# Optimization experiments

Measured on AMD Instinct MI355X. Metric: run time of the kernel, lower is better.

Reference implementation:

```python
import jax, jax.numpy as jnp
import numpy as np

N = 50000
E = 800000
F_IN = 128
HID = 60
CAT = 3 * HID
NUM_CLASSES = 7
EPS = 1e-5


def _gcn_norm(edge_index, n):
    # add self loops, symmetric normalization (PyG gcn_norm default)
    loops = jnp.arange(n, dtype=edge_index.dtype)
    src = jnp.concatenate([edge_index[0], loops])
    dst = jnp.concatenate([edge_index[1], loops])
    deg = jax.ops.segment_sum(jnp.ones_like(src, dtype=jnp.float32), dst, num_segments=n)
    dinv = jnp.where(deg > 0, jax.lax.rsqrt(jnp.maximum(deg, 1.0)), 0.0)
    norm = dinv[src] * dinv[dst]  # [E+N]
    return src, dst, norm


def _prop(x, src, dst, norm, n):
    # sum_{j in N(i)} norm_ij * x_j
    return jax.ops.segment_sum(x[src] * norm[:, None], dst, num_segments=n)


def _mixhop(x, src, dst, norm, n, ws, bs):
    outs = [x @ ws[0] + bs[0]]  # power 0
    h = x
    for w, b in zip(ws[1:], bs[1:]):  # powers 1, 2
        h = _prop(h, src, dst, norm, n)
        outs.append(h @ w + b)
    return jnp.concatenate(outs, axis=-1)


def _batchnorm(x, g, b):
    # training-mode batch stats over node dim (biased variance, eps=1e-5)
    mu = x.mean(axis=0)
    var = x.var(axis=0)
    return (x - mu) * jax.lax.rsqrt(var + EPS) * g + b


def setup_inputs() -> dict:
    key = jax.random.key(0)
    ks = jax.random.split(key, 16)
    x = jax.random.normal(ks[0], (N, F_IN), dtype=jnp.float32)
    edge_index = jax.random.randint(ks[1], (2, E), 0, N, dtype=jnp.int64)
    def lin(k, fi, fo):
        s = 1.0 / np.sqrt(fi)
        return jax.random.uniform(k, (fi, fo), jnp.float32, -s, s)
    inp = {"x": x, "edge_index": edge_index}
    for i, p in enumerate(range(3)):
        inp[f"c1_w{p}"] = lin(ks[2 + p], F_IN, HID)
        inp[f"c1_b{p}"] = jnp.zeros((HID,), jnp.float32)
        inp[f"c2_w{p}"] = lin(ks[5 + p], CAT, HID)
        inp[f"c2_b{p}"] = jnp.zeros((HID,), jnp.float32)
        inp[f"c3_w{p}"] = lin(ks[8 + p], CAT, HID)
        inp[f"c3_b{p}"] = jnp.zeros((HID,), jnp.float32)
    for i in (1, 2, 3):
        inp[f"bn{i}_g"] = jnp.ones((CAT,), jnp.float32)
        inp[f"bn{i}_b"] = jnp.zeros((CAT,), jnp.float32)
    inp["lin_w"] = lin(ks[11], CAT, NUM_CLASSES)
    inp["lin_b"] = jnp.zeros((NUM_CLASSES,), jnp.float32)
    return inp


def reference(x, edge_index,
              c1_w0, c1_b0, c1_w1, c1_b1, c1_w2, c1_b2,
              c2_w0, c2_b0, c2_w1, c2_b1, c2_w2, c2_b2,
              c3_w0, c3_b0, c3_w1, c3_b1, c3_w2, c3_b2,
              bn1_g, bn1_b, bn2_g, bn2_b, bn3_g, bn3_b,
              lin_w, lin_b):
    n = x.shape[0]
    src, dst, norm = _gcn_norm(edge_index, n)
    # dropout layers are identity in eval mode
    h = _mixhop(x, src, dst, norm, n, (c1_w0, c1_w1, c1_w2), (c1_b0, c1_b1, c1_b2))
    h = _batchnorm(h, bn1_g, bn1_b)
    h = _mixhop(h, src, dst, norm, n, (c2_w0, c2_w1, c2_w2), (c2_b0, c2_b1, c2_b2))
    h = _batchnorm(h, bn2_g, bn2_b)
    h = _mixhop(h, src, dst, norm, n, (c3_w0, c3_w1, c3_w2), (c3_b0, c3_b1, c3_b2))
    h = _batchnorm(h, bn3_g, bn3_b)
    return h @ lin_w + lin_b
```

## Files before the change

kernel.cpp:

```cpp
#include <hip/hip_runtime.h>
#include <hip/hip_bf16.h>

#define NN 50000
#define NE 800000
#define FIN0 128
#define HID 60
#define CAT 180
#define NCLS 7
#define BN_EPS 1e-5f
#define NBUCK 196
#define BCAP 5120
#define STG 96

typedef unsigned int uint;
typedef unsigned short ushort;
typedef __attribute__((ext_vector_type(8))) short short8;
typedef __attribute__((ext_vector_type(4))) float f32x4;

__device__ __forceinline__ ushort f2bf(float f) {
    uint u = __float_as_uint(f);
    u += 0x7FFFu + ((u >> 16) & 1u);
    return (ushort)(u >> 16);
}
__device__ __forceinline__ float bf_lo(uint v) { return __uint_as_float(v << 16); }
__device__ __forceinline__ float bf_hi(uint v) { return __uint_as_float(v & 0xFFFF0000u); }
__device__ __forceinline__ float bf2f(ushort u) { return __uint_as_float(((uint)u) << 16); }


__global__ void k_initcur(int* __restrict__ gcur) {
    int t = threadIdx.x;
    if (t < NBUCK) gcur[t] = t * BCAP;
}

__global__ __launch_bounds__(256) void k_bin(const int* __restrict__ src,
                                             const int* __restrict__ dst,
                                             int* __restrict__ gcur,
                                             uint* __restrict__ ebuf, int e) {
    __shared__ int cnt[NBUCK];
    __shared__ int base[NBUCK];
    int t = threadIdx.x;
    for (int c0 = blockIdx.x * 2048; c0 < e; c0 += gridDim.x * 2048) {
        if (t < NBUCK) cnt[t] = 0;
        __syncthreads();
        uint pe[8]; int rk[8], bk[8], ok[8];
#pragma unroll
        for (int j = 0; j < 8; ++j) {
            int i = c0 + j * 256 + t;
            ok[j] = i < e;
            if (ok[j]) {
                int sv = src[i], dv = dst[i];
                pe[j] = (uint)(sv & 0xFFFF) | ((uint)(dv & 255) << 16);
                bk[j] = dv >> 8;
                rk[j] = atomicAdd(&cnt[bk[j]], 1);
            }
        }
        __syncthreads();
        if (t < NBUCK && cnt[t] > 0) base[t] = atomicAdd(&gcur[t], cnt[t]);
        __syncthreads();
#pragma unroll
        for (int j = 0; j < 8; ++j) {
            if (ok[j]) ebuf[base[bk[j]] + rk[j]] = pe[j];
        }
        __syncthreads();
    }
}

__global__ void k_bscan(const int* __restrict__ gcur, int* __restrict__ bbase,
                        int* __restrict__ bcnt, int* __restrict__ row_ptr) {
    __shared__ int s[256];
    int t = threadIdx.x;
    int c = (t < NBUCK) ? (gcur[t] - t * BCAP) : 0;
    s[t] = c;
    __syncthreads();
    for (int off = 1; off < 256; off <<= 1) {
        int v = (t >= off) ? s[t - off] : 0;
        __syncthreads();
        s[t] += v;
        __syncthreads();
    }
    if (t < NBUCK) { bbase[t] = s[t] - c; bcnt[t] = c; }
    if (t == 0) row_ptr[NN] = NE;
}

__global__ __launch_bounds__(256) void k_bucket_csr(
        const uint* __restrict__ ebuf, const int* __restrict__ bbase,
        const int* __restrict__ bcnt,
        int* __restrict__ row_ptr, float* __restrict__ dinv,
        ushort* __restrict__ ssrc, int n) {
    __shared__ int ncnt[256];
    __shared__ int loff[256];
    int b = blockIdx.x, t = threadIdx.x;
    int cnt = bcnt[b];
    int gbase = bbase[b];
    const uint* ee = ebuf + (size_t)b * BCAP;
    ncnt[t] = 0;
    __syncthreads();
    for (int i = t; i < cnt; i += 256) atomicAdd(&ncnt[(ee[i] >> 16) & 255], 1);
    __syncthreads();
    int c = ncnt[t];
    loff[t] = c;
    __syncthreads();
    for (int off = 1; off < 256; off <<= 1) {
        int v = (t >= off) ? loff[t - off] : 0;
        __syncthreads();
        loff[t] += v;
        __syncthreads();
    }
    int excl = loff[t] - c;
    int node = b * 256 + t;
    if (node < n) {
        row_ptr[node] = gbase + excl;
        dinv[node] = rsqrtf((float)(c + 1));
    }
    __syncthreads();
    ncnt[t] = excl;
    __syncthreads();
    for (int i = t; i < cnt; i += 256) {
        uint pe = ee[i];
        int pos = atomicAdd(&ncnt[(pe >> 16) & 255], 1);
        ssrc[gbase + pos] = (ushort)(pe & 0xFFFF);
    }
}

__global__ void k_wpack_all(
        const float* __restrict__ w00, const float* __restrict__ w01, const float* __restrict__ w02,
        const float* __restrict__ w10, const float* __restrict__ w11, const float* __restrict__ w12,
        const float* __restrict__ w20, const float* __restrict__ w21, const float* __restrict__ w22,
        ushort* __restrict__ WP0, ushort* __restrict__ WP1, ushort* __restrict__ WP2) {
    int l = blockIdx.z, p = blockIdx.y;
    int kt = blockIdx.x >> 2, ct = blockIdx.x & 3;
    int KT = (l == 0) ? 4 : 6;
    if (kt >= KT) return;
    const float* W;
    if (l == 0) W = (p == 0) ? w00 : ((p == 1) ? w01 : w02);
    else if (l == 1) W = (p == 0) ? w10 : ((p == 1) ? w11 : w12);
    else W = (p == 0) ? w20 : ((p == 1) ? w21 : w22);
    ushort* WP = (l == 0) ? WP0 : ((l == 1) ? WP1 : WP2);
    int lane = threadIdx.x;
    int k0 = kt * 32 + (lane >> 4) * 8;
    int c = ct * 16 + (lane & 15);
    ushort* dst = WP + (((size_t)(p * KT + kt) * 4 + ct) << 9) + (lane << 3);
    ushort o[8];
#pragma unroll
    for (int j = 0; j < 8; ++j) {
        int kl = k0 + j;
        float v = 0.f;
        if (c < 60) {
            if (l == 0) {
                if (kl < FIN0) v = W[(size_t)kl * 60 + c];
            } else {
                int rgn = kl >> 6, cc = kl & 63;
                if (cc < 60) v = W[(size_t)(rgn * 60 + cc) * 60 + c];
            }
        }
        o[j] = f2bf(v);
    }
    *(ushort4*)dst = make_ushort4(o[0], o[1], o[2], o[3]);
    *(ushort4*)(dst + 4) = make_ushort4(o[4], o[5], o[6], o[7]);
}

template <int KT, int MODE>
__global__ __launch_bounds__(256) void k_gemm_mfma(
        const float* __restrict__ Xf,
        const ushort* __restrict__ B0q, const ushort* __restrict__ B1q,
        const ushort* __restrict__ B2q,
        const float* __restrict__ gsum, const float* __restrict__ gsum2,
        const float* __restrict__ bng, const float* __restrict__ bnb,
        const ushort* __restrict__ WP,
        const float* __restrict__ b0, const float* __restrict__ dinv,
        ushort* __restrict__ Y0, ushort* __restrict__ Y12, int n) {
    __shared__ float ssc[200], ssh[200];
    const int t = threadIdx.x;
    if (MODE == 1) {
        if (t < 192) {
            int rgn = t >> 6, cc = t & 63;
            float sc = 0.f, sh = 0.f;
            if (cc < 60) {
                int c = rgn * 60 + cc;
                float mu = gsum[c] / (float)n;
                float var = gsum2[c] / (float)n - mu * mu;
                sc = rsqrtf(var + BN_EPS) * bng[c];
                sh = bnb[c] - mu * sc;
            }
            ssc[t] = sc; ssh[t] = sh;
        }
        __syncthreads();
    }
    const int wv = t >> 6;
    const int lane = t & 63;
    const int l15 = lane & 15;
    const int lhi = lane >> 4;
    const int nb = blockIdx.x * 64 + wv * 16;

    f32x4 acc[3][4];
#pragma unroll
    for (int p = 0; p < 3; ++p)
#pragma unroll
        for (int ct = 0; ct < 4; ++ct) acc[p][ct] = (f32x4){0.f, 0.f, 0.f, 0.f};

    const int arow = nb + l15;
    const int arowc = (arow < n) ? arow : 0;
    const ushort* wpL = WP + (lane << 3);

#pragma unroll
    for (int kt = 0; kt < KT; ++kt) {
        short8 a;
        if (MODE == 0) {
            const float* xr = Xf + (size_t)arowc * (KT * 32) + kt * 32 + lhi * 8;
            float4 v0 = *(const float4*)xr;
            float4 v1 = *(const float4*)(xr + 4);
            a[0] = (short)f2bf(v0.x); a[1] = (short)f2bf(v0.y);
            a[2] = (short)f2bf(v0.z); a[3] = (short)f2bf(v0.w);
            a[4] = (short)f2bf(v1.x); a[5] = (short)f2bf(v1.y);
            a[6] = (short)f2bf(v1.z); a[7] = (short)f2bf(v1.w);
        } else {
            const ushort* base = (kt < 2) ? B0q : ((kt < 4) ? B1q : B2q);
            const ushort* ar = base + (size_t)arowc * 64 + (kt & 1) * 32 + lhi * 8;
            uint4 raw = *(const uint4*)ar;
            int kb = kt * 32 + lhi * 8;
            float4 sc0 = *(const float4*)&ssc[kb];
            float4 sc1 = *(const float4*)&ssc[kb + 4];
            float4 sh0 = *(const float4*)&ssh[kb];
            float4 sh1 = *(const float4*)&ssh[kb + 4];
            a[0] = (short)f2bf(bf_lo(raw.x) * sc0.x + sh0.x);
            a[1] = (short)f2bf(bf_hi(raw.x) * sc0.y + sh0.y);
            a[2] = (short)f2bf(bf_lo(raw.y) * sc0.z + sh0.z);
            a[3] = (short)f2bf(bf_hi(raw.y) * sc0.w + sh0.w);
            a[4] = (short)f2bf(bf_lo(raw.z) * sc1.x + sh1.x);
            a[5] = (short)f2bf(bf_hi(raw.z) * sc1.y + sh1.y);
            a[6] = (short)f2bf(bf_lo(raw.w) * sc1.z + sh1.z);
            a[7] = (short)f2bf(bf_hi(raw.w) * sc1.w + sh1.w);
        }
#pragma unroll
        for (int p = 0; p < 3; ++p)
#pragma unroll
            for (int ct = 0; ct < 4; ++ct) {
                short8 b = *(const short8*)(wpL + (((size_t)(p * KT + kt) * 4 + ct) << 9));
                acc[p][ct] = __builtin_amdgcn_mfma_f32_16x16x32_bf16(a, b, acc[p][ct], 0, 0, 0);
            }
    }

    float dv[4];
#pragma unroll
    for (int j = 0; j < 4; ++j) {
        int node = nb + lhi * 4 + j;
        dv[j] = (node < n) ? dinv[node] : 0.f;
    }
#pragma unroll
    for (int ct = 0; ct < 4; ++ct) {
        int col = ct * 16 + l15;
        if (col >= 60) continue;
        float bias = b0[col];
#pragma unroll
        for (int j = 0; j < 4; ++j) {
            int node = nb + lhi * 4 + j;
            if (node >= n) continue;
            Y0[(size_t)node * 64 + col] = f2bf(acc[0][ct][j] + bias);
            uint pk = ((uint)f2bf(dv[j] * acc[2][ct][j]) << 16) |
                      (uint)f2bf(dv[j] * acc[1][ct][j]);
            *(uint*)(Y12 + (size_t)node * 128 + 2 * col) = pk;
        }
    }
}

__global__ __launch_bounds__(256) void k_propA(
        const ushort* __restrict__ Y12, ushort* __restrict__ Z1, ushort* __restrict__ ZQ,
        const float* __restrict__ b1,
        const float* __restrict__ dinv, const int* __restrict__ rp,
        const ushort* __restrict__ es, int n) {
    __shared__ ushort sidx[4][STG];
    int sub = threadIdx.x >> 6;
    int lane = threadIdx.x & 63;
    int node = blockIdx.x * 4 + sub;
    if (node >= n) return;
    int e0 = rp[node], e1 = rp[node + 1];
    int deg = e1 - e0;
    int stg = (deg < STG) ? deg : STG;
    for (int i = lane; i < stg; i += 64) sidx[sub][i] = es[e0 + i];
    if (lane >= 60) return;
    uint sv = *(const uint*)(Y12 + (size_t)node * 128 + 2 * lane);
    float a1 = bf_lo(sv);
    float a2 = bf_hi(sv);
    int e = 0;
    for (; e + 15 < stg; e += 16) {
        uint v[16];
#pragma unroll
        for (int j = 0; j < 16; ++j) {
            int s = sidx[sub][e + j];
            v[j] = *(const uint*)(Y12 + (size_t)s * 128 + 2 * lane);
        }
#pragma unroll
        for (int j = 0; j < 16; ++j) { a1 += bf_lo(v[j]); a2 += bf_hi(v[j]); }
    }
    for (; e + 3 < stg; e += 4) {
        uint v[4];
#pragma unroll
        for (int j = 0; j < 4; ++j) {
            int s = sidx[sub][e + j];
            v[j] = *(const uint*)(Y12 + (size_t)s * 128 + 2 * lane);
        }
#pragma unroll
        for (int j = 0; j < 4; ++j) { a1 += bf_lo(v[j]); a2 += bf_hi(v[j]); }
    }
    for (; e < stg; ++e) {
        uint v = *(const uint*)(Y12 + (size_t)sidx[sub][e] * 128 + 2 * lane);
        a1 += bf_lo(v);
        a2 += bf_hi(v);
    }
    for (int ee = e0 + stg; ee < e1; ++ee) {
        uint v = *(const uint*)(Y12 + (size_t)es[ee] * 128 + 2 * lane);
        a1 += bf_lo(v);
        a2 += bf_hi(v);
    }
    float di = dinv[node];
    Z1[(size_t)node * 64 + lane] = f2bf(di * a1 + b1[lane]);
    ZQ[(size_t)node * 64 + lane] = f2bf(di * di * a2);
}

__global__ __launch_bounds__(256) void k_propB(
        const ushort* __restrict__ ZQ, ushort* __restrict__ Q2,
        const float* __restrict__ b2,
        const float* __restrict__ dinv, const int* __restrict__ rp,
        const ushort* __restrict__ es, int n) {
    __shared__ ushort sidx[4][STG];
    int sub = threadIdx.x >> 6;
    int lane = threadIdx.x & 63;
    int node = blockIdx.x * 4 + sub;
    if (node >= n) return;
    int e0 = rp[node], e1 = rp[node + 1];
    int deg = e1 - e0;
    int stg = (deg < STG) ? deg : STG;
    for (int i = lane; i < stg; i += 64) sidx[sub][i] = es[e0 + i];
    if (lane >= 60) return;
    float acc = bf2f(ZQ[(size_t)node * 64 + lane]);
    int e = 0;
    for (; e + 15 < stg; e += 16) {
        ushort v[16];
#pragma unroll
        for (int j = 0; j < 16; ++j) {
            int s = sidx[sub][e + j];
            v[j] = ZQ[(size_t)s * 64 + lane];
        }
#pragma unroll
        for (int j = 0; j < 16; ++j) acc += bf2f(v[j]);
    }
    for (; e + 3 < stg; e += 4) {
        ushort v[4];
#pragma unroll
        for (int j = 0; j < 4; ++j) {
            int s = sidx[sub][e + j];
            v[j] = ZQ[(size_t)s * 64 + lane];
        }
#pragma unroll
        for (int j = 0; j < 4; ++j) acc += bf2f(v[j]);
    }
    for (; e < stg; ++e) acc += bf2f(ZQ[(size_t)sidx[sub][e] * 64 + lane]);
    for (int ee = e0 + stg; ee < e1; ++ee) acc += bf2f(ZQ[(size_t)es[ee] * 64 + lane]);
    Q2[(size_t)node * 64 + lane] = f2bf(dinv[node] * acc + b2[lane]);
}

__global__ __launch_bounds__(256) void k_bnstats(
        const ushort* __restrict__ Y0, const ushort* __restrict__ Z1,
        const ushort* __restrict__ Q2,
        float* __restrict__ gsum, float* __restrict__ gsum2, int n) {
    int rgn = blockIdx.y;
    const ushort* __restrict__ src = (rgn == 0) ? Y0 : ((rgn == 1) ? Z1 : Q2);
    int t = threadIdx.x;
    int c8 = (t & 7) * 8;
    int rsub = t >> 3;
    float s1[8], s2[8];
#pragma unroll
    for (int j = 0; j < 8; ++j) { s1[j] = 0.f; s2[j] = 0.f; }
    for (int r = blockIdx.x * 32 + rsub; r < n; r += gridDim.x * 32) {
        uint4 v = *(const uint4*)(src + (size_t)r * 64 + c8);
        float f;
        f = bf_lo(v.x); s1[0] += f; s2[0] += f * f;
        f = bf_hi(v.x); s1[1] += f; s2[1] += f * f;
        f = bf_lo(v.y); s1[2] += f; s2[2] += f * f;
        f = bf_hi(v.y); s1[3] += f; s2[3] += f * f;
        f = bf_lo(v.z); s1[4] += f; s2[4] += f * f;
        f = bf_hi(v.z); s1[5] += f; s2[5] += f * f;
        f = bf_lo(v.w); s1[6] += f; s2[6] += f * f;
        f = bf_hi(v.w); s1[7] += f; s2[7] += f * f;
    }
#pragma unroll
    for (int m = 8; m < 64; m <<= 1) {
#pragma unroll
        for (int j = 0; j < 8; ++j) {
            s1[j] += __shfl_xor(s1[j], m);
            s2[j] += __shfl_xor(s2[j], m);
        }
    }
    __shared__ float ls1[4][64], ls2[4][64];
    int wv = t >> 6, lane = t & 63;
    if (lane < 8) {
#pragma unroll
        for (int j = 0; j < 8; ++j) {
            ls1[wv][lane * 8 + j] = s1[j];
            ls2[wv][lane * 8 + j] = s2[j];
        }
    }
    __syncthreads();
    if (t < 60) {
        float a1 = ls1[0][t] + ls1[1][t] + ls1[2][t] + ls1[3][t];
        float a2 = ls2[0][t] + ls2[1][t] + ls2[2][t] + ls2[3][t];
        atomicAdd(&gsum[rgn * 60 + t], a1);
        atomicAdd(&gsum2[rgn * 60 + t], a2);
    }
}

__global__ __launch_bounds__(256) void k_final_fused(
        const ushort* __restrict__ Y0, const ushort* __restrict__ Z1,
        const ushort* __restrict__ Q2,
        const float* __restrict__ gsum, const float* __restrict__ gsum2,
        const float* __restrict__ g, const float* __restrict__ bb,
        const float* __restrict__ w, const float* __restrict__ wb,
        float* __restrict__ out, int n) {
    __shared__ float sw[CAT * NCLS];
    __shared__ float ssc[CAT], ssh[CAT];
    __shared__ float sb[NCLS];
    int t = threadIdx.x;
    for (int i = t; i < CAT * NCLS; i += 256) sw[i] = w[i];
    if (t < CAT) {
        float mu = gsum[t] / (float)n;
        float var = gsum2[t] / (float)n - mu * mu;
        float sc = rsqrtf(var + BN_EPS) * g[t];
        ssc[t] = sc;
        ssh[t] = bb[t] - mu * sc;
    }
    if (t < NCLS) sb[t] = wb[t];
    __syncthreads();
    int node = blockIdx.x * 256 + t;
    if (node >= n) return;
    float acc[NCLS];
#pragma unroll
    for (int j = 0; j < NCLS; ++j) acc[j] = sb[j];
    const ushort* bufs[3] = {Y0, Z1, Q2};
#pragma unroll
    for (int rgn = 0; rgn < 3; ++rgn) {
        const ushort* sp = bufs[rgn] + (size_t)node * 64;
        int cb = rgn * 60;
#pragma unroll 6
        for (int k2 = 0; k2 < 30; ++k2) {
            uint u = *(const uint*)(sp + 2 * k2);
            int c = cb + 2 * k2;
            float f0 = bf_lo(u) * ssc[c] + ssh[c];
            float f1 = bf_hi(u) * ssc[c + 1] + ssh[c + 1];
#pragma unroll
            for (int j = 0; j < NCLS; ++j)
                acc[j] += f0 * sw[c * NCLS + j] + f1 * sw[(c + 1) * NCLS + j];
        }
    }
#pragma unroll
    for (int j = 0; j < NCLS; ++j) out[(size_t)node * NCLS + j] = acc[j];
}

extern "C" void kernel_launch(void* const* d_in, const int* in_sizes, int n_in,
                              void* d_out, int out_size, void* d_ws, size_t ws_size,
                              hipStream_t stream) {
    const float* x = (const float*)d_in[0];
    const int* ei = (const int*)d_in[1];
    const int* esrc = ei;
    const int* edst = ei + NE;

    const float* c_w[3][3];
    const float* c_b[3][3];
    for (int p = 0; p < 3; ++p)
        for (int l = 0; l < 3; ++l) {
            c_w[l][p] = (const float*)d_in[2 + p * 6 + l * 2];
            c_b[l][p] = (const float*)d_in[3 + p * 6 + l * 2];
        }
    const float* bn_g[3] = {(const float*)d_in[20], (const float*)d_in[22], (const float*)d_in[24]};
    const float* bn_b[3] = {(const float*)d_in[21], (const float*)d_in[23], (const float*)d_in[25]};
    const float* lw = (const float*)d_in[26];
    const float* lb = (const float*)d_in[27];
    float* out = (float*)d_out;

    char* wp = (char*)d_ws;
    auto alloc = [&](size_t bytes) {
        char* p = wp;
        wp += (bytes + 255) & ~(size_t)255;
        return p;
    };
    int* gcur = (int*)alloc((size_t)NBUCK * 4);
    int* bbase = (int*)alloc((size_t)(NBUCK + 1) * 4);
    int* bcnt = (int*)alloc((size_t)NBUCK * 4);
    uint* ebuf = (uint*)alloc((size_t)NBUCK * BCAP * 4);
    int* row_ptr = (int*)alloc((size_t)(NN + 1) * 4);
    ushort* ssrc = (ushort*)alloc((size_t)NE * 2);
    float* dinv = (float*)alloc((size_t)NN * 4);
    float* gsumAll = (float*)alloc((size_t)3 * 2 * CAT * 4);
    ushort* Y0 = (ushort*)alloc((size_t)NN * 64 * 2);
    ushort* Y12 = (ushort*)alloc((size_t)NN * 128 * 2);
    ushort* Z1 = (ushort*)alloc((size_t)NN * 64 * 2);
    ushort* ZQ = (ushort*)alloc((size_t)NN * 64 * 2);
    ushort* Q2 = (ushort*)alloc((size_t)NN * 64 * 2);
    ushort* WP1 = (ushort*)alloc((size_t)3 * 4 * 4 * 512 * 2);
    ushort* WP2 = (ushort*)alloc((size_t)3 * 6 * 4 * 512 * 2);
    ushort* WP3 = (ushort*)alloc((size_t)3 * 6 * 4 * 512 * 2);

    auto gs = [&](int l) { return gsumAll + (size_t)l * 2 * CAT; };
    auto gs2 = [&](int l) { return gsumAll + (size_t)l * 2 * CAT + CAT; };

    k_initcur<<<1, 256, 0, stream>>>(gcur);
    k_bin<<<391, 256, 0, stream>>>(esrc, edst, gcur, ebuf, NE);
    k_bscan<<<1, 256, 0, stream>>>(gcur, bbase, bcnt, row_ptr);
    k_bucket_csr<<<NBUCK, 256, 0, stream>>>(ebuf, bbase, bcnt, row_ptr, dinv, ssrc, NN);

    k_wpack_all<<<dim3(24, 3, 3), 64, 0, stream>>>(
        c_w[0][0], c_w[0][1], c_w[0][2],
        c_w[1][0], c_w[1][1], c_w[1][2],
        c_w[2][0], c_w[2][1], c_w[2][2],
        WP1, WP2, WP3);
    hipMemsetAsync(gsumAll, 0, (size_t)3 * 2 * CAT * 4, stream);

    const int gemm_gx = (NN + 63) / 64;
    const int prop_gx = (NN + 3) / 4;

    for (int l = 0; l < 3; ++l) {
        if (l == 0) {
            k_gemm_mfma<4, 0><<<gemm_gx, 256, 0, stream>>>(
                x, nullptr, nullptr, nullptr, nullptr, nullptr, nullptr, nullptr,
                WP1, c_b[0][0], dinv, Y0, Y12, NN);
        } else {
            const ushort* WPl = (l == 1) ? WP2 : WP3;
            k_gemm_mfma<6, 1><<<gemm_gx, 256, 0, stream>>>(
                nullptr, Y0, Z1, Q2, gs(l - 1), gs2(l - 1), bn_g[l - 1], bn_b[l - 1],
                WPl, c_b[l][0], dinv, Y0, Y12, NN);
        }
        k_propA<<<prop_gx, 256, 0, stream>>>(Y12, Z1, ZQ, c_b[l][1], dinv, row_ptr, ssrc, NN);
        k_propB<<<prop_gx, 256, 0, stream>>>(ZQ, Q2, c_b[l][2], dinv, row_ptr, ssrc, NN);
        k_bnstats<<<dim3(256, 3), 256, 0, stream>>>(Y0, Z1, Q2, gs(l), gs2(l), NN);
    }

    k_final_fused<<<(NN + 255) / 256, 256, 0, stream>>>(
        Y0, Z1, Q2, gs(2), gs2(2), bn_g[2], bn_b[2], lw, lb, out, NN);
}
```

Measured before the change: 332.1 us.

## Use half-wave per node in propagation with wider loads and double-buffered gathers

The propagation kernels now give each node 32 lanes, each handling two or four bf16 columns with wider uint/uint2 loads, so eight nodes share a 256-thread block instead of four. The 16-edge gather batches are double-buffered, so the next batch's loads are issued before the current one is accumulated. Separately, the initcur kernel, the bucket scan kernel and the memset are folded into the weight-pack and bucket-CSR kernels to cut launch count. The risks are higher register pressure from the two gather buffers and a 256-element scan that every CSR block now repeats.

```diff
diff --git a/kernel.cpp b/kernel.cpp
--- a/kernel.cpp
+++ b/kernel.cpp
@@ -26,109 +26,21 @@
 __device__ __forceinline__ float bf_hi(uint v) { return __uint_as_float(v & 0xFFFF0000u); }
 __device__ __forceinline__ float bf2f(ushort u) { return __uint_as_float(((uint)u) << 16); }
 
-
-__global__ void k_initcur(int* __restrict__ gcur) {
-    int t = threadIdx.x;
-    if (t < NBUCK) gcur[t] = t * BCAP;
-}
-
-__global__ __launch_bounds__(256) void k_bin(const int* __restrict__ src,
-                                             const int* __restrict__ dst,
-                                             int* __restrict__ gcur,
-                                             uint* __restrict__ ebuf, int e) {
-    __shared__ int cnt[NBUCK];
-    __shared__ int base[NBUCK];
-    int t = threadIdx.x;
-    for (int c0 = blockIdx.x * 2048; c0 < e; c0 += gridDim.x * 2048) {
-        if (t < NBUCK) cnt[t] = 0;
-        __syncthreads();
-        uint pe[8]; int rk[8], bk[8], ok[8];
-#pragma unroll
-        for (int j = 0; j < 8; ++j) {
-            int i = c0 + j * 256 + t;
-            ok[j] = i < e;
-            if (ok[j]) {
-                int sv = src[i], dv = dst[i];
-                pe[j] = (uint)(sv & 0xFFFF) | ((uint)(dv & 255) << 16);
-                bk[j] = dv >> 8;
-                rk[j] = atomicAdd(&cnt[bk[j]], 1);
-            }
-        }
-        __syncthreads();
-        if (t < NBUCK && cnt[t] > 0) base[t] = atomicAdd(&gcur[t], cnt[t]);
-        __syncthreads();
-#pragma unroll
-        for (int j = 0; j < 8; ++j) {
-            if (ok[j]) ebuf[base[bk[j]] + rk[j]] = pe[j];
-        }
-        __syncthreads();
-    }
-}
-
-__global__ void k_bscan(const int* __restrict__ gcur, int* __restrict__ bbase,
-                        int* __restrict__ bcnt, int* __restrict__ row_ptr) {
-    __shared__ int s[256];
-    int t = threadIdx.x;
-    int c = (t < NBUCK) ? (gcur[t] - t * BCAP) : 0;
-    s[t] = c;
-    __syncthreads();
-    for (int off = 1; off < 256; off <<= 1) {
-        int v = (t >= off) ? s[t - off] : 0;
-        __syncthreads();
-        s[t] += v;
-        __syncthreads();
-    }
-    if (t < NBUCK) { bbase[t] = s[t] - c; bcnt[t] = c; }
-    if (t == 0) row_ptr[NN] = NE;
-}
-
-__global__ __launch_bounds__(256) void k_bucket_csr(
-        const uint* __restrict__ ebuf, const int* __restrict__ bbase,
-        const int* __restrict__ bcnt,
-        int* __restrict__ row_ptr, float* __restrict__ dinv,
-        ushort* __restrict__ ssrc, int n) {
-    __shared__ int ncnt[256];
-    __shared__ int loff[256];
-    int b = blockIdx.x, t = threadIdx.x;
-    int cnt = bcnt[b];
-    int gbase = bbase[b];
-    const uint* ee = ebuf + (size_t)b * BCAP;
-    ncnt[t] = 0;
-    __syncthreads();
-    for (int i = t; i < cnt; i += 256) atomicAdd(&ncnt[(ee[i] >> 16) & 255], 1);
-    __syncthreads();
-    int c = ncnt[t];
-    loff[t] = c;
-    __syncthreads();
-    for (int off = 1; off < 256; off <<= 1) {
-        int v = (t >= off) ? loff[t - off] : 0;
-        __syncthreads();
-        loff[t] += v;
-        __syncthreads();
-    }
-    int excl = loff[t] - c;
-    int node = b * 256 + t;
-    if (node < n) {
-        row_ptr[node] = gbase + excl;
-        dinv[node] = rsqrtf((float)(c + 1));
-    }
-    __syncthreads();
-    ncnt[t] = excl;
-    __syncthreads();
-    for (int i = t; i < cnt; i += 256) {
-        uint pe = ee[i];
-        int pos = atomicAdd(&ncnt[(pe >> 16) & 255], 1);
-        ssrc[gbase + pos] = (ushort)(pe & 0xFFFF);
-    }
-}
-
 __global__ void k_wpack_all(
         const float* __restrict__ w00, const float* __restrict__ w01, const float* __restrict__ w02,
         const float* __restrict__ w10, const float* __restrict__ w11, const float* __restrict__ w12,
         const float* __restrict__ w20, const float* __restrict__ w21, const float* __restrict__ w22,
-        ushort* __restrict__ WP0, ushort* __restrict__ WP1, ushort* __restrict__ WP2) {
+        ushort* __restrict__ WP0, ushort* __restrict__ WP1, ushort* __restrict__ WP2,
+        int* __restrict__ gcur, float* __restrict__ gsumAll) {
     int l = blockIdx.z, p = blockIdx.y;
     int kt = blockIdx.x >> 2, ct = blockIdx.x & 3;
+    int lane = threadIdx.x;
+    if (l == 0 && p == 0 && blockIdx.x == 0) {
+        for (int i = lane; i < NBUCK; i += 64) gcur[i] = i * BCAP;
+    }
+    if (l == 0 && p == 1 && blockIdx.x == 0) {
+        for (int i = lane; i < 3 * 2 * CAT; i += 64) gsumAll[i] = 0.f;
+    }
     int KT = (l == 0) ? 4 : 6;
     if (kt >= KT) return;
     const float* W;
@@ -136,7 +48,6 @@
     else if (l == 1) W = (p == 0) ? w10 : ((p == 1) ? w11 : w12);
     else W = (p == 0) ? w20 : ((p == 1) ? w21 : w22);
     ushort* WP = (l == 0) ? WP0 : ((l == 1) ? WP1 : WP2);
-    int lane = threadIdx.x;
     int k0 = kt * 32 + (lane >> 4) * 8;
     int c = ct * 16 + (lane & 15);
     ushort* dst = WP + (((size_t)(p * KT + kt) * 4 + ct) << 9) + (lane << 3);
@@ -157,6 +68,89 @@
     }
     *(ushort4*)dst = make_ushort4(o[0], o[1], o[2], o[3]);
     *(ushort4*)(dst + 4) = make_ushort4(o[4], o[5], o[6], o[7]);
+}
+
+__global__ __launch_bounds__(256) void k_bin(const int* __restrict__ src,
+                                             const int* __restrict__ dst,
+                                             int* __restrict__ gcur,
+                                             uint* __restrict__ ebuf, int e) {
+    __shared__ int cnt[NBUCK];
+    __shared__ int base[NBUCK];
+    int t = threadIdx.x;
+    for (int c0 = blockIdx.x * 2048; c0 < e; c0 += gridDim.x * 2048) {
+        if (t < NBUCK) cnt[t] = 0;
+        __syncthreads();
+        uint pe[8]; int rk[8], bk[8], ok[8];
+#pragma unroll
+        for (int j = 0; j < 8; ++j) {
+            int i = c0 + j * 256 + t;
+            ok[j] = i < e;
+            if (ok[j]) {
+                int sv = src[i], dv = dst[i];
+                pe[j] = (uint)(sv & 0xFFFF) | ((uint)(dv & 255) << 16);
+                bk[j] = dv >> 8;
+                rk[j] = atomicAdd(&cnt[bk[j]], 1);
+            }
+        }
+        __syncthreads();
+        if (t < NBUCK && cnt[t] > 0) base[t] = atomicAdd(&gcur[t], cnt[t]);
+        __syncthreads();
+#pragma unroll
+        for (int j = 0; j < 8; ++j) {
+            if (ok[j]) ebuf[base[bk[j]] + rk[j]] = pe[j];
+        }
+        __syncthreads();
+    }
+}
+
+__global__ __launch_bounds__(256) void k_bucket_csr(
+        const int* __restrict__ gcur, const uint* __restrict__ ebuf,
+        int* __restrict__ row_ptr, float* __restrict__ dinv,
+        ushort* __restrict__ ssrc, int n) {
+    __shared__ int sc[256];
+    __shared__ int ncnt[256];
+    __shared__ int loff[256];
+    int b = blockIdx.x, t = threadIdx.x;
+    int cbt = (t < NBUCK) ? (gcur[t] - t * BCAP) : 0;
+    sc[t] = cbt;
+    __syncthreads();
+    for (int off = 1; off < 256; off <<= 1) {
+        int v = (t >= off) ? sc[t - off] : 0;
+        __syncthreads();
+        sc[t] += v;
+        __syncthreads();
+    }
+    int gbase = (b == 0) ? 0 : sc[b - 1];
+    int cnt = sc[b] - gbase;
+    if (b == 0 && t == 0) row_ptr[NN] = NE;
+    const uint* ee = ebuf + (size_t)b * BCAP;
+    ncnt[t] = 0;
+    __syncthreads();
+    for (int i = t; i < cnt; i += 256) atomicAdd(&ncnt[(ee[i] >> 16) & 255], 1);
+    __syncthreads();
+    int c = ncnt[t];
+    loff[t] = c;
+    __syncthreads();
+    for (int off = 1; off < 256; off <<= 1) {
+        int v = (t >= off) ? loff[t - off] : 0;
+        __syncthreads();
+        loff[t] += v;
+        __syncthreads();
+    }
+    int excl = loff[t] - c;
+    int node = b * 256 + t;
+    if (node < n) {
+        row_ptr[node] = gbase + excl;
+        dinv[node] = rsqrtf((float)(c + 1));
+    }
+    __syncthreads();
+    ncnt[t] = excl;
+    __syncthreads();
+    for (int i = t; i < cnt; i += 256) {
+        uint pe = ee[i];
+        int pos = atomicAdd(&ncnt[(pe >> 16) & 255], 1);
+        ssrc[gbase + pos] = (ushort)(pe & 0xFFFF);
+    }
 }
 
 template <int KT, int MODE>
@@ -268,53 +262,73 @@
         const float* __restrict__ b1,
         const float* __restrict__ dinv, const int* __restrict__ rp,
         const ushort* __restrict__ es, int n) {
-    __shared__ ushort sidx[4][STG];
-    int sub = threadIdx.x >> 6;
-    int lane = threadIdx.x & 63;
-    int node = blockIdx.x * 4 + sub;
+    __shared__ ushort sidx[8][STG];
+    int sub = threadIdx.x >> 5;
+    int hl = threadIdx.x & 31;
+    int node = blockIdx.x * 8 + sub;
     if (node >= n) return;
     int e0 = rp[node], e1 = rp[node + 1];
     int deg = e1 - e0;
     int stg = (deg < STG) ? deg : STG;
-    for (int i = lane; i < stg; i += 64) sidx[sub][i] = es[e0 + i];
-    if (lane >= 60) return;
-    uint sv = *(const uint*)(Y12 + (size_t)node * 128 + 2 * lane);
-    float a1 = bf_lo(sv);
-    float a2 = bf_hi(sv);
-    int e = 0;
-    for (; e + 15 < stg; e += 16) {
-        uint v[16];
-#pragma unroll
-        for (int j = 0; j < 16; ++j) {
-            int s = sidx[sub][e + j];
-            v[j] = *(const uint*)(Y12 + (size_t)s * 128 + 2 * lane);
-        }
-#pragma unroll
-        for (int j = 0; j < 16; ++j) { a1 += bf_lo(v[j]); a2 += bf_hi(v[j]); }
-    }
+    for (int i = hl; i < stg; i += 32) sidx[sub][i] = es[e0 + i];
+    if (hl >= 30) return;
+    uint2 sv = *(const uint2*)(Y12 + (size_t)node * 128 + hl * 4);
+    float a1x = bf_lo(sv.x), a2x = bf_hi(sv.x);
+    float a1y = bf_lo(sv.y), a2y = bf_hi(sv.y);
+#define LOADA(buf, base)                                                      \
+    _Pragma("unroll") for (int j = 0; j < 16; ++j) {                          \
+        int s = sidx[sub][(base) + j];                                        \
+        buf[j] = *(const uint2*)(Y12 + (size_t)s * 128 + hl * 4);             \
+    }
+#define ACCA(buf)                                                             \
+    _Pragma("unroll") for (int j = 0; j < 16; ++j) {                          \
+        a1x += bf_lo(buf[j].x); a2x += bf_hi(buf[j].x);                       \
+        a1y += bf_lo(buf[j].y); a2y += bf_hi(buf[j].y);                       \
+    }
+    int nfull = stg >> 4;
+    uint2 va[16], vb[16];
+    if (nfull > 0) LOADA(va, 0);
+    for (int c = 0; c < nfull; ++c) {
+        if (c & 1) {
+            if (c + 1 < nfull) LOADA(va, (c + 1) * 16);
+            ACCA(vb);
+        } else {
+            if (c + 1 < nfull) LOADA(vb, (c + 1) * 16);
+            ACCA(va);
+        }
+    }
+    int e = nfull * 16;
     for (; e + 3 < stg; e += 4) {
-        uint v[4];
+        uint2 v[4];
 #pragma unroll
         for (int j = 0; j < 4; ++j) {
             int s = sidx[sub][e + j];
-            v[j] = *(const uint*)(Y12 + (size_t)s * 128 + 2 * lane);
-        }
-#pragma unroll
-        for (int j = 0; j < 4; ++j) { a1 += bf_lo(v[j]); a2 += bf_hi(v[j]); }
+            v[j] = *(const uint2*)(Y12 + (size_t)s * 128 + hl * 4);
+        }
+#pragma unroll
+        for (int j = 0; j < 4; ++j) {
+            a1x += bf_lo(v[j].x); a2x += bf_hi(v[j].x);
+            a1y += bf_lo(v[j].y); a2y += bf_hi(v[j].y);
+        }
     }
     for (; e < stg; ++e) {
-        uint v = *(const uint*)(Y12 + (size_t)sidx[sub][e] * 128 + 2 * lane);
-        a1 += bf_lo(v);
-        a2 += bf_hi(v);
+        uint2 v = *(const uint2*)(Y12 + (size_t)sidx[sub][e] * 128 + hl * 4);
+        a1x += bf_lo(v.x); a2x += bf_hi(v.x);
+        a1y += bf_lo(v.y); a2y += bf_hi(v.y);
     }
     for (int ee = e0 + stg; ee < e1; ++ee) {
-        uint v = *(const uint*)(Y12 + (size_t)es[ee] * 128 + 2 * lane);
-        a1 += bf_lo(v);
-        a2 += bf_hi(v);
-    }
+        uint2 v = *(const uint2*)(Y12 + (size_t)es[ee] * 128 + hl * 4);
+        a1x += bf_lo(v.x); a2x += bf_hi(v.x);
+        a1y += bf_lo(v.y); a2y += bf_hi(v.y);
+    }
+#undef LOADA
+#undef ACCA
     float di = dinv[node];
-    Z1[(size_t)node * 64 + lane] = f2bf(di * a1 + b1[lane]);
-    ZQ[(size_t)node * 64 + lane] = f2bf(di * di * a2);
+    int c0 = 2 * hl;
+    uint z1 = ((uint)f2bf(di * a1y + b1[c0 + 1]) << 16) | (uint)f2bf(di * a1x + b1[c0]);
+    uint zq = ((uint)f2bf(di * di * a2y) << 16) | (uint)f2bf(di * di * a2x);
+    *(uint*)(Z1 + (size_t)node * 64 + c0) = z1;
+    *(uint*)(ZQ + (size_t)node * 64 + c0) = zq;
 }
 
 __global__ __launch_bounds__(256) void k_propB(
@@ -322,41 +336,64 @@
         const float* __restrict__ b2,
         const float* __restrict__ dinv, const int* __restrict__ rp,
         const ushort* __restrict__ es, int n) {
-    __shared__ ushort sidx[4][STG];
-    int sub = threadIdx.x >> 6;
-    int lane = threadIdx.x & 63;
-    int node = blockIdx.x * 4 + sub;
+    __shared__ ushort sidx[8][STG];
+    int sub = threadIdx.x >> 5;
+    int hl = threadIdx.x & 31;
+    int node = blockIdx.x * 8 + sub;
     if (node >= n) return;
     int e0 = rp[node], e1 = rp[node + 1];
     int deg = e1 - e0;
     int stg = (deg < STG) ? deg : STG;
-    for (int i = lane; i < stg; i += 64) sidx[sub][i] = es[e0 + i];
-    if (lane >= 60) return;
-    float acc = bf2f(ZQ[(size_t)node * 64 + lane]);
-    int e = 0;
-    for (; e + 15 < stg; e += 16) {
-        ushort v[16];
-#pragma unroll
-        for (int j = 0; j < 16; ++j) {
-            int s = sidx[sub][e + j];
-            v[j] = ZQ[(size_t)s * 64 + lane];
-        }
-#pragma unroll
-        for (int j = 0; j < 16; ++j) acc += bf2f(v[j]);
-    }
+    for (int i = hl; i < stg; i += 32) sidx[sub][i] = es[e0 + i];
+    if (hl >= 30) return;
+    uint sv = *(const uint*)(ZQ + (size_t)node * 64 + 2 * hl);
+    float ax = bf_lo(sv), ay = bf_hi(sv);
+#define LOADB(buf, base)                                                      \
+    _Pragma("unroll") for (int j = 0; j < 16; ++j) {                          \
+        int s = sidx[sub][(base) + j];                                        \
+        buf[j] = *(const uint*)(ZQ + (size_t)s * 64 + 2 * hl);                \
+    }
+#define ACCB(buf)                                                             \
+    _Pragma("unroll") for (int j = 0; j < 16; ++j) {                          \
+        ax += bf_lo(buf[j]); ay += bf_hi(buf[j]);                             \
+    }
+    int nfull = stg >> 4;
+    uint va[16], vb[16];
+    if (nfull > 0) LOADB(va, 0);
+    for (int c = 0; c < nfull; ++c) {
+        if (c & 1) {
+            if (c + 1 < nfull) LOADB(va, (c + 1) * 16);
+            ACCB(vb);
+        } else {
+            if (c + 1 < nfull) LOADB(vb, (c + 1) * 16);
+            ACCB(va);
+        }
+    }
+    int e = nfull * 16;
     for (; e + 3 < stg; e += 4) {
-        ushort v[4];
+        uint v[4];
 #pragma unroll
         for (int j = 0; j < 4; ++j) {
             int s = sidx[sub][e + j];
-            v[j] = ZQ[(size_t)s * 64 + lane];
-        }
-#pragma unroll
-        for (int j = 0; j < 4; ++j) acc += bf2f(v[j]);
-    }
-    for (; e < stg; ++e) acc += bf2f(ZQ[(size_t)sidx[sub][e] * 64 + lane]);
-    for (int ee = e0 + stg; ee < e1; ++ee) acc += bf2f(ZQ[(size_t)es[ee] * 64 + lane]);
-    Q2[(size_t)node * 64 + lane] = f2bf(dinv[node] * acc + b2[lane]);
+            v[j] = *(const uint*)(ZQ + (size_t)s * 64 + 2 * hl);
+        }
+#pragma unroll
+        for (int j = 0; j < 4; ++j) { ax += bf_lo(v[j]); ay += bf_hi(v[j]); }
+    }
+    for (; e < stg; ++e) {
+        uint v = *(const uint*)(ZQ + (size_t)sidx[sub][e] * 64 + 2 * hl);
+        ax += bf_lo(v); ay += bf_hi(v);
+    }
+    for (int ee = e0 + stg; ee < e1; ++ee) {
+        uint v = *(const uint*)(ZQ + (size_t)es[ee] * 64 + 2 * hl);
+        ax += bf_lo(v); ay += bf_hi(v);
+    }
+#undef LOADB
+#undef ACCB
+    float di = dinv[node];
+    int c0 = 2 * hl;
+    uint q = ((uint)f2bf(di * ay + b2[c0 + 1]) << 16) | (uint)f2bf(di * ax + b2[c0]);
+    *(uint*)(Q2 + (size_t)node * 64 + c0) = q;
 }
 
 __global__ __launch_bounds__(256) void k_bnstats(
@@ -483,8 +520,6 @@
         return p;
     };
     int* gcur = (int*)alloc((size_t)NBUCK * 4);
-    int* bbase = (int*)alloc((size_t)(NBUCK + 1) * 4);
-    int* bcnt = (int*)alloc((size_t)NBUCK * 4);
     uint* ebuf = (uint*)alloc((size_t)NBUCK * BCAP * 4);
     int* row_ptr = (int*)alloc((size_t)(NN + 1) * 4);
     ushort* ssrc = (ushort*)alloc((size_t)NE * 2);
@@ -502,20 +537,17 @@
     auto gs = [&](int l) { return gsumAll + (size_t)l * 2 * CAT; };
     auto gs2 = [&](int l) { return gsumAll + (size_t)l * 2 * CAT + CAT; };
 
-    k_initcur<<<1, 256, 0, stream>>>(gcur);
-    k_bin<<<391, 256, 0, stream>>>(esrc, edst, gcur, ebuf, NE);
-    k_bscan<<<1, 256, 0, stream>>>(gcur, bbase, bcnt, row_ptr);
-    k_bucket_csr<<<NBUCK, 256, 0, stream>>>(ebuf, bbase, bcnt, row_ptr, dinv, ssrc, NN);
-
     k_wpack_all<<<dim3(24, 3, 3), 64, 0, stream>>>(
         c_w[0][0], c_w[0][1], c_w[0][2],
         c_w[1][0], c_w[1][1], c_w[1][2],
         c_w[2][0], c_w[2][1], c_w[2][2],
-        WP1, WP2, WP3);
-    hipMemsetAsync(gsumAll, 0, (size_t)3 * 2 * CAT * 4, stream);
+        WP1, WP2, WP3, gcur, gsumAll);
+
+    k_bin<<<391, 256, 0, stream>>>(esrc, edst, gcur, ebuf, NE);
+    k_bucket_csr<<<NBUCK, 256, 0, stream>>>(gcur, ebuf, row_ptr, dinv, ssrc, NN);
 
     const int gemm_gx = (NN + 63) / 64;
-    const int prop_gx = (NN + 3) / 4;
+    const int prop_gx = (NN + 7) / 8;
 
     for (int l = 0; l < 3; ++l) {
         if (l == 0) {
```

Result: slower. 362.5 us (+9.2%).
